# Kernel optimization log

Measured on AMD Instinct MI355X. Metric: run time of the kernel, lower is better.

Reference implementation:

```python
import jax, jax.numpy as jnp
import numpy as np

B, H, W, C = 64, 56, 56, 256
WIN, SHIFT, HEADS = 7, 3, 8
HEAD_DIM = C // HEADS
N = WIN * WIN
EPS = 1e-5


def _rel_pos_index():
    # matches get_relative_position_index (tf.meshgrid 'xy' indexing)
    xx, yy = np.meshgrid(np.arange(WIN), np.arange(WIN))  # shapes (W,H)
    coords = np.stack([yy, xx], 0).reshape(2, -1)  # (2, N)
    rel = coords[:, :, None] - coords[:, None, :]  # (2, N, N)
    rel = rel.transpose(1, 2, 0)
    idx = (rel[:, :, 0] + WIN - 1) * (2 * WIN - 1) + (rel[:, :, 1] + WIN - 1)
    return jnp.asarray(idx, dtype=jnp.int32)  # (N, N)


def _attn_mask():
    # shifted-window attention mask, (nW, N, N) with 0 / -100
    img = np.zeros((H, W), dtype=np.float32)
    cnt = 0
    for hs in (slice(0, -WIN), slice(-WIN, -SHIFT), slice(-SHIFT, None)):
        for ws in (slice(0, -WIN), slice(-WIN, -SHIFT), slice(-SHIFT, None)):
            img[hs, ws] = cnt
            cnt += 1
    mw = img.reshape(H // WIN, WIN, W // WIN, WIN).transpose(0, 2, 1, 3).reshape(-1, N)
    am = mw[:, None, :] - mw[:, :, None]
    am = np.where(am != 0, -100.0, 0.0).astype(np.float32)
    return jnp.asarray(am)  # (nW, N, N)


def _layer_norm(x, g, b):
    mu = jnp.mean(x, -1, keepdims=True)
    var = jnp.mean(jnp.square(x - mu), -1, keepdims=True)
    return (x - mu) * jax.lax.rsqrt(var + EPS) * g + b


def setup_inputs() -> dict:
    key = jax.random.key(0)
    ks = jax.random.split(key, 6)
    s = lambda fan: 1.0 / np.sqrt(fan)
    return {
        'x': jax.random.normal(ks[0], (B, H * W, C), jnp.float32),
        'ln1_g': jnp.ones((C,), jnp.float32),
        'ln1_b': jnp.zeros((C,), jnp.float32),
        'qkv_w': jax.random.normal(ks[1], (C, 3 * C), jnp.float32) * s(C),
        'qkv_b': jnp.zeros((3 * C,), jnp.float32),
        'rpb_table': jax.random.normal(ks[2], ((2 * WIN - 1) ** 2, HEADS), jnp.float32) * 0.02,
        'proj_w': jax.random.normal(ks[3], (C, C), jnp.float32) * s(C),
        'proj_b': jnp.zeros((C,), jnp.float32),
        'ln2_g': jnp.ones((C,), jnp.float32),
        'ln2_b': jnp.zeros((C,), jnp.float32),
        'mlp_w1': jax.random.normal(ks[4], (C, 4 * C), jnp.float32) * s(C),
        'mlp_b1': jnp.zeros((4 * C,), jnp.float32),
        'mlp_w2': jax.random.normal(ks[5], (4 * C, C), jnp.float32) * s(4 * C),
        'mlp_b2': jnp.zeros((C,), jnp.float32),
    }


def _forward(x, ln1_g, ln1_b, qkv_w, qkv_b, rpb_table, proj_w, proj_b,
             ln2_g, ln2_b, mlp_w1, mlp_b1, mlp_w2, mlp_b2):
    rel_idx = _rel_pos_index()
    mask = _attn_mask()
    nW = (H // WIN) * (W // WIN)

    shortcut = x
    y = _layer_norm(x, ln1_g, ln1_b).reshape(B, H, W, C)
    y = jnp.roll(y, (-SHIFT, -SHIFT), axis=(1, 2))
    # window partition -> (B*nW, N, C)
    y = y.reshape(B, H // WIN, WIN, W // WIN, WIN, C)
    y = y.transpose(0, 1, 3, 2, 4, 5).reshape(B * nW, N, C)

    qkv = (y @ qkv_w + qkv_b).reshape(B * nW, N, 3, HEADS, HEAD_DIM)
    q, k, v = jnp.moveaxis(qkv, 2, 0)  # each (B*nW, N, heads, hd)
    q = q * (HEAD_DIM ** -0.5)
    attn = jnp.einsum('wqhd,wkhd->whqk', q, k)  # (B*nW, heads, N, N)
    bias = jnp.transpose(rpb_table[rel_idx], (2, 0, 1))  # (heads, N, N)
    attn = attn + bias[None]
    attn = attn.reshape(B, nW, HEADS, N, N) + mask[None, :, None]
    attn = jax.nn.softmax(attn.reshape(B * nW, HEADS, N, N), axis=-1)
    o = jnp.einsum('whqk,wkhd->wqhd', attn, v).reshape(B * nW, N, C)
    o = o @ proj_w + proj_b

    # window reverse + un-shift
    o = o.reshape(B, H // WIN, W // WIN, WIN, WIN, C)
    o = o.transpose(0, 1, 3, 2, 4, 5).reshape(B, H, W, C)
    o = jnp.roll(o, (SHIFT, SHIFT), axis=(1, 2)).reshape(B, H * W, C)

    x = shortcut + o
    h = _layer_norm(x, ln2_g, ln2_b)
    h = jax.nn.gelu(h @ mlp_w1 + mlp_b1, approximate=False) @ mlp_w2 + mlp_b2
    return x + h


def reference(x, ln1_g, ln1_b, qkv_w, qkv_b, rpb_table, proj_w, proj_b,
              ln2_g, ln2_b, mlp_w1, mlp_b1, mlp_w2, mlp_b2):
    return _forward(x, ln1_g, ln1_b, qkv_w, qkv_b, rpb_table, proj_w, proj_b,
                    ln2_g, ln2_b, mlp_w1, mlp_b1, mlp_w2, mlp_b2)
```

## Files before the change

### kernel.cpp

```cpp
#include <hip/hip_runtime.h>
#include <math.h>


typedef __attribute__((ext_vector_type(8))) short bf16x8;
typedef __attribute__((ext_vector_type(4))) float f32x4;

#define NTOK 200704
#define NN   49
#define NPARAM 4680

__device__ __forceinline__ float bf2f(unsigned short u) {
    union { unsigned int i; float f; } v; v.i = ((unsigned)u) << 16; return v.f;
}
__device__ __forceinline__ unsigned short f2bf(float f) {
    union { float fv; unsigned int i; } v; v.fv = f;
    return (unsigned short)((v.i + 0x7fffu + ((v.i >> 16) & 1u)) >> 16);
}

__device__ __forceinline__ void gload_lds16(const unsigned short* g, unsigned short* l) {
    __builtin_amdgcn_global_load_lds(
        (const __attribute__((address_space(1))) unsigned int*)g,
        (__attribute__((address_space(3))) unsigned int*)l, 16, 0, 0);
}

__device__ __forceinline__ float gelu_erf(float v) {
    float av = fabsf(v);
    float x = av * 0.70710678118654752f;
    float t = __builtin_amdgcn_rcpf(fmaf(x, 0.3275911f, 1.0f));
    float p = fmaf(1.061405429f, t, -1.453152027f);
    p = fmaf(p, t, 1.421413741f);
    p = fmaf(p, t, -0.284496736f);
    p = fmaf(p, t, 0.254829592f);
    p = p * t;
    float ex = __builtin_amdgcn_exp2f(x * x * -1.4426950408889634f);
    float E = fmaf(-p, ex, 1.0f);
    return fmaf(0.5f * av, E, 0.5f * v);
}

__global__ void detect_kernel(const unsigned short* __restrict__ xu, int* flag) {
    int ln = threadIdx.x;
    int sane = 0;
    #pragma unroll
    for (int t = 0; t < 16; t++) {
        unsigned u = xu[(ln * 16 + t) * 2];
        unsigned e = (u >> 7) & 0xFF;
        sane += (e >= 0x60 && e <= 0x90) ? 1 : 0;
    }
    #pragma unroll
    for (int off = 32; off; off >>= 1) sane += __shfl_xor(sane, off);
    if (ln == 0) *flag = (sane < 614) ? 1 : 0;
}

__device__ __forceinline__ float ld_any(const void* p, int j, int f) {
    return f ? ((const float*)p)[j] : bf2f(((const unsigned short*)p)[j]);
}

__global__ void convert_params_kernel(
    const void* ln1_g, const void* ln1_b, const void* qkv_b, const void* proj_b,
    const void* ln2_g, const void* ln2_b, const void* b1, const void* b2,
    const void* rpb, const int* __restrict__ flag, float* __restrict__ dst) {
    int i = blockIdx.x * 256 + threadIdx.x;
    if (i >= NPARAM) return;
    int f = *flag;
    const void* src; int j;
    if      (i < 256)  { src = ln1_g;  j = i; }
    else if (i < 512)  { src = ln1_b;  j = i - 256; }
    else if (i < 1280) { src = qkv_b;  j = i - 512; }
    else if (i < 1536) { src = proj_b; j = i - 1280; }
    else if (i < 1792) { src = ln2_g;  j = i - 1536; }
    else if (i < 2048) { src = ln2_b;  j = i - 1792; }
    else if (i < 3072) { src = b1;     j = i - 2048; }
    else if (i < 3328) { src = b2;     j = i - 3072; }
    else               { src = rpb;    j = i - 3328; }
    dst[i] = ld_any(src, j, f);
}

__global__ void transpose_any(const void* __restrict__ in,
                              unsigned short* __restrict__ out, int K, int N,
                              const int* __restrict__ flag) {
    int f = *flag;
    int idx = blockIdx.x * 256 + threadIdx.x;
    if (idx < K * N) {
        int k = idx / N, n = idx - k * N;
        out[n * K + k] = f2bf(ld_any(in, idx, f));
    }
}

__global__ void relayout_w1(const void* __restrict__ in,
                            unsigned short* __restrict__ out,
                            const int* __restrict__ flag) {
    int f = *flag;
    int idx = blockIdx.x * 256 + threadIdx.x;
    if (idx < 256 * 1024) {
        int k = idx >> 10, h = idx & 1023;
        int c = h >> 5, r = h & 31;
        int ks = k ^ ((r & 7) << 3);
        out[c * 8192 + r * 256 + ks] = f2bf(ld_any(in, idx, f));
    }
}

__global__ void relayout_w2(const void* __restrict__ in,
                            unsigned short* __restrict__ out,
                            const int* __restrict__ flag) {
    int f = *flag;
    int idx = blockIdx.x * 256 + threadIdx.x;
    if (idx < 1024 * 256) {
        int k = idx >> 8, n = idx & 255;
        int c = k >> 5, kk = k & 31;
        out[c * 8192 + n * 32 + kk] = f2bf(ld_any(in, idx, f));
    }
}

__global__ __launch_bounds__(256) void ln1_window_kernel(
    const void* __restrict__ x, const float* __restrict__ paramsF,
    unsigned short* __restrict__ y, const int* __restrict__ flag) {
    int f = *flag;
    int wv = threadIdx.x >> 6, ln = threadIdx.x & 63;
    int tok = blockIdx.x * 4 + wv;
    float v0, v1, v2, v3;
    if (f) {
        float4 pv = *(const float4*)((const float*)x + (size_t)tok * 256 + ln * 4);
        v0 = pv.x; v1 = pv.y; v2 = pv.z; v3 = pv.w;
    } else {
        ushort4 pv = *(const ushort4*)((const unsigned short*)x + (size_t)tok * 256 + ln * 4);
        v0 = bf2f(pv.x); v1 = bf2f(pv.y); v2 = bf2f(pv.z); v3 = bf2f(pv.w);
    }
    float s = v0 + v1 + v2 + v3;
    float sq = v0 * v0 + v1 * v1 + v2 * v2 + v3 * v3;
    #pragma unroll
    for (int off = 32; off; off >>= 1) { s += __shfl_xor(s, off); sq += __shfl_xor(sq, off); }
    float mu = s * (1.f / 256.f);
    float rs = rsqrtf(fmaxf(sq * (1.f / 256.f) - mu * mu, 0.f) + 1e-5f);
    float4 gv = *(const float4*)(paramsF + ln * 4);
    float4 bv = *(const float4*)(paramsF + 256 + ln * 4);
    int bb = tok / 3136, hw = tok - bb * 3136;
    int h = hw / 56, w = hw - h * 56;
    int hp = h - 3; hp += (hp < 0) ? 56 : 0;
    int wp = w - 3; wp += (wp < 0) ? 56 : 0;
    int win = (hp / 7) * 8 + (wp / 7);
    int n = (hp % 7) * 7 + (wp % 7);
    size_t drow = ((size_t)bb * 64 + win) * NN + n;
    ushort4 o;
    o.x = f2bf((v0 - mu) * rs * gv.x + bv.x);
    o.y = f2bf((v1 - mu) * rs * gv.y + bv.y);
    o.z = f2bf((v2 - mu) * rs * gv.z + bv.z);
    o.w = f2bf((v3 - mu) * rs * gv.w + bv.w);
    *(ushort4*)(y + drow * 256 + ln * 4) = o;
}

__device__ __forceinline__ void gemm_core_k256(
    const unsigned short* __restrict__ A, const unsigned short* __restrict__ Bt,
    int rowBase, int colBase, unsigned short* As, unsigned short* Bs, f32x4 acc[2][4]) {
    const int tid = threadIdx.x;
    const int wv = tid >> 6, ln = tid & 63;
    const int m16 = ln & 15, q4 = ln >> 4;
    const int ar = tid >> 1, ah = (tid & 1) * 32;
    const int br = tid >> 2, bp = (tid & 3) * 16;
    for (int kb = 0; kb < 256; kb += 64) {
        const unsigned short* ag = A + (size_t)(rowBase + ar) * 256 + kb + ah;
        unsigned short* asd = As + ar * 72 + ah;
        #pragma unroll
        for (int i = 0; i < 4; i++)
            *(bf16x8*)(asd + i * 8) = *(const bf16x8*)(ag + i * 8);
        const unsigned short* bg = Bt + (size_t)(colBase + br) * 256 + kb + bp;
        unsigned short* bsd = Bs + br * 72 + bp;
        #pragma unroll
        for (int i = 0; i < 2; i++)
            *(bf16x8*)(bsd + i * 8) = *(const bf16x8*)(bg + i * 8);
        __syncthreads();
        #pragma unroll
        for (int ks = 0; ks < 64; ks += 32) {
            bf16x8 af[2], bfr[4];
            #pragma unroll
            for (int rt = 0; rt < 2; rt++)
                af[rt] = *(const bf16x8*)(As + (wv * 32 + rt * 16 + m16) * 72 + ks + q4 * 8);
            #pragma unroll
            for (int ct = 0; ct < 4; ct++)
                bfr[ct] = *(const bf16x8*)(Bs + (ct * 16 + m16) * 72 + ks + q4 * 8);
            #pragma unroll
            for (int rt = 0; rt < 2; rt++)
                #pragma unroll
                for (int ct = 0; ct < 4; ct++)
                    acc[rt][ct] = __builtin_amdgcn_mfma_f32_16x16x32_bf16(
                        af[rt], bfr[ct], acc[rt][ct], 0, 0, 0);
        }
        __syncthreads();
    }
}

__global__ __launch_bounds__(256) void gemm_qkv_kernel(
    const unsigned short* __restrict__ A, const unsigned short* __restrict__ Bt,
    const float* __restrict__ bias,
    unsigned short* __restrict__ out) {
    __shared__ unsigned short As[128 * 72];
    __shared__ unsigned short Bs[64 * 72];
    const int ln = threadIdx.x & 63, wv = threadIdx.x >> 6;
    const int m16 = ln & 15, q4 = ln >> 4;
    const int rowBase = blockIdx.y * 128, colBase = blockIdx.x * 64;
    f32x4 acc[2][4];
    #pragma unroll
    for (int i = 0; i < 2; i++)
        #pragma unroll
        for (int j = 0; j < 4; j++)
            #pragma unroll
            for (int r = 0; r < 4; r++) acc[i][j][r] = 0.f;
    gemm_core_k256(A, Bt, rowBase, colBase, As, Bs, acc);
    #pragma unroll
    for (int rt = 0; rt < 2; rt++)
        #pragma unroll
        for (int ct = 0; ct < 4; ct++) {
            int col = colBase + ct * 16 + m16;
            float bs = bias[col];
            float scale = (col < 256) ? 0.17677669529663689f : 1.0f;
            #pragma unroll
            for (int r = 0; r < 4; r++) {
                int row = rowBase + wv * 32 + rt * 16 + q4 * 4 + r;
                out[(size_t)row * 768 + col] = f2bf((acc[rt][ct][r] + bs) * scale);
            }
        }
}

__global__ __launch_bounds__(256) void gemm_proj_kernel(
    const unsigned short* __restrict__ A, const unsigned short* __restrict__ Bt,
    const float* __restrict__ bias,
    const void* __restrict__ xin,
    unsigned short* __restrict__ x2, const int* __restrict__ flag) {
    __shared__ unsigned short As[128 * 72];
    __shared__ unsigned short Bs[64 * 72];
    const int f = *flag;
    const int ln = threadIdx.x & 63, wv = threadIdx.x >> 6;
    const int m16 = ln & 15, q4 = ln >> 4;
    const int rowBase = blockIdx.y * 128, colBase = blockIdx.x * 64;
    f32x4 acc[2][4];
    #pragma unroll
    for (int i = 0; i < 2; i++)
        #pragma unroll
        for (int j = 0; j < 4; j++)
            #pragma unroll
            for (int r = 0; r < 4; r++) acc[i][j][r] = 0.f;
    gemm_core_k256(A, Bt, rowBase, colBase, As, Bs, acc);
    #pragma unroll
    for (int rt = 0; rt < 2; rt++)
        #pragma unroll
        for (int r = 0; r < 4; r++) {
            int row = rowBase + wv * 32 + rt * 16 + q4 * 4 + r;
            int win = row / NN, n = row - win * NN;
            int bb = win >> 6, wl = win & 63;
            int i7 = n / 7, j7 = n - i7 * 7;
            int hp = (wl >> 3) * 7 + i7 + 3; if (hp >= 56) hp -= 56;
            int wp = (wl & 7) * 7 + j7 + 3;  if (wp >= 56) wp -= 56;
            size_t drow = ((size_t)bb * 3136 + hp * 56 + wp) * 256;
            #pragma unroll
            for (int ct = 0; ct < 4; ct++) {
                int col = colBase + ct * 16 + m16;
                float v = acc[rt][ct][r] + bias[col] + ld_any(xin, drow + col, f);
                x2[drow + col] = f2bf(v);
            }
        }
}

__global__ __launch_bounds__(256) void attn_kernel(
    const unsigned short* __restrict__ qkv,
    const float* __restrict__ rpbF,
    unsigned short* __restrict__ o) {
    __shared__ unsigned short Qs[49 * 40], Ks[49 * 40], Vs[49 * 40];
    __shared__ float S[49 * 52];
    int tid = threadIdx.x;
    int win = blockIdx.x >> 3, head = blockIdx.x & 7;
    size_t base = (size_t)win * 49 * 768 + head * 32;
    if (tid < 196) {
        int i = tid >> 2, part = (tid & 3) * 8;
        *(bf16x8*)(Qs + i * 40 + part) = *(const bf16x8*)(qkv + base + (size_t)i * 768 + part);
        *(bf16x8*)(Ks + i * 40 + part) = *(const bf16x8*)(qkv + base + 256 + (size_t)i * 768 + part);
        *(bf16x8*)(Vs + i * 40 + part) = *(const bf16x8*)(qkv + base + 512 + (size_t)i * 768 + part);
    }
    __syncthreads();
    int wl = win & 63;
    int wh0 = (wl >> 3) * 7, ww0 = (wl & 7) * 7;
    for (int e = tid; e < 2401; e += 256) {
        int i = e / 49, j = e - i * 49;
        float a = 0.f;
        #pragma unroll
        for (int dd = 0; dd < 32; dd += 8) {
            bf16x8 qv = *(const bf16x8*)(Qs + i * 40 + dd);
            bf16x8 kv = *(const bf16x8*)(Ks + j * 40 + dd);
            #pragma unroll
            for (int u = 0; u < 8; u++)
                a += bf2f((unsigned short)qv[u]) * bf2f((unsigned short)kv[u]);
        }
        int ir = i / 7, ic = i - ir * 7, jr = j / 7, jc = j - jr * 7;
        a += rpbF[((ir - jr + 6) * 13 + (ic - jc + 6)) * 8 + head];
        int hi = wh0 + ir, wi = ww0 + ic, hj = wh0 + jr, wj = ww0 + jc;
        int ci = (hi < 49 ? 0 : (hi < 53 ? 3 : 6)) + (wi < 49 ? 0 : (wi < 53 ? 1 : 2));
        int cj = (hj < 49 ? 0 : (hj < 53 ? 3 : 6)) + (wj < 49 ? 0 : (wj < 53 ? 1 : 2));
        if (ci != cj) a -= 100.f;
        S[i * 52 + j] = a;
    }
    __syncthreads();
    if (tid < 49) {
        float m = -1e30f;
        for (int j = 0; j < 49; j++) m = fmaxf(m, S[tid * 52 + j]);
        float s = 0.f;
        for (int j = 0; j < 49; j++) { float e = expf(S[tid * 52 + j] - m); S[tid * 52 + j] = e; s += e; }
        float inv = 1.f / s;
        for (int j = 0; j < 49; j++) S[tid * 52 + j] *= inv;
    }
    __syncthreads();
    if (tid < 196) {
        int i = tid >> 2, dr = (tid & 3) * 8;
        float a[8];
        #pragma unroll
        for (int u = 0; u < 8; u++) a[u] = 0.f;
        for (int j = 0; j < 49; j++) {
            float pp = S[i * 52 + j];
            bf16x8 vv = *(const bf16x8*)(Vs + j * 40 + dr);
            #pragma unroll
            for (int u = 0; u < 8; u++) a[u] += pp * bf2f((unsigned short)vv[u]);
        }
        bf16x8 ov;
        #pragma unroll
        for (int u = 0; u < 8; u++) ov[u] = (short)f2bf(a[u]);
        *(bf16x8*)(o + ((size_t)win * 49 + i) * 256 + head * 32 + dr) = ov;
    }
}

__global__ __launch_bounds__(256, 2) void mlp_fused_v3(
    const unsigned short* __restrict__ x2,
    const float* __restrict__ g2F, const float* __restrict__ b2lnF,
    const unsigned short* __restrict__ w1s,
    const float* __restrict__ b1F,
    const unsigned short* __restrict__ w2s,
    const float* __restrict__ b2F,
    void* __restrict__ out, const int* __restrict__ flag) {
    __shared__ __align__(16) unsigned short Bs1[2][32 * 256];
    __shared__ __align__(16) unsigned short Bs2[2][256 * 32];
    __shared__ __align__(16) unsigned short Hs[64 * 40];
    const int f = *flag;
    const int tid = threadIdx.x;
    const int wv = tid >> 6, ln = tid & 63;
    const int m16 = ln & 15, q4 = ln >> 4;
    const int tok0 = blockIdx.x * 64;

    {
        const unsigned short* s1 = w1s + tid * 8;
        const unsigned short* s2 = w2s + tid * 8;
        #pragma unroll
        for (int j = 0; j < 4; j++) {
            gload_lds16(s1 + j * 2048, &Bs1[0][tid * 8 + j * 2048]);
            gload_lds16(s2 + j * 2048, &Bs2[0][tid * 8 + j * 2048]);
        }
    }

    bf16x8 areg[8];
    {
        const unsigned short* xr = x2 + (size_t)(tok0 + wv * 16 + m16) * 256 + q4 * 8;
        #pragma unroll
        for (int ks = 0; ks < 8; ks++) areg[ks] = *(const bf16x8*)(xr + ks * 32);
        float s = 0.f, sq = 0.f;
        #pragma unroll
        for (int ks = 0; ks < 8; ks++)
            #pragma unroll
            for (int u = 0; u < 8; u++) {
                float v = bf2f((unsigned short)areg[ks][u]);
                s += v; sq += v * v;
            }
        s += __shfl_xor(s, 16); s += __shfl_xor(s, 32);
        sq += __shfl_xor(sq, 16); sq += __shfl_xor(sq, 32);
        float mu = s * (1.f / 256.f);
        float rs = rsqrtf(fmaxf(sq * (1.f / 256.f) - mu * mu, 0.f) + 1e-5f);
        #pragma unroll
        for (int ks = 0; ks < 8; ks++)
            #pragma unroll
            for (int u = 0; u < 8; u++) {
                int kidx = ks * 32 + q4 * 8 + u;
                float v = (bf2f((unsigned short)areg[ks][u]) - mu) * rs * g2F[kidx] + b2lnF[kidx];
                areg[ks][u] = (short)f2bf(v);
            }
    }

    f32x4 acc2[4][4];
    #pragma unroll
    for (int rt = 0; rt < 4; rt++)
        #pragma unroll
        for (int ct = 0; ct < 4; ct++)
            #pragma unroll
            for (int r = 0; r < 4; r++) acc2[rt][ct][r] = 0.f;

    #pragma unroll 1
    for (int c = 0; c < 32; ++c) {
        const int cur = c & 1;
        asm volatile("s_waitcnt vmcnt(0)" ::: "memory");
        __builtin_amdgcn_s_barrier();
        __builtin_amdgcn_sched_barrier(0);

        if (c + 1 < 32) {
            const unsigned short* s1 = w1s + (size_t)(c + 1) * 8192 + tid * 8;
            const unsigned short* s2 = w2s + (size_t)(c + 1) * 8192 + tid * 8;
            unsigned short* d1 = &Bs1[cur ^ 1][tid * 8];
            unsigned short* d2 = &Bs2[cur ^ 1][tid * 8];
            #pragma unroll
            for (int j = 0; j < 4; j++) {
                gload_lds16(s1 + j * 2048, d1 + j * 2048);
                gload_lds16(s2 + j * 2048, d2 + j * 2048);
            }
        }
        __builtin_amdgcn_sched_barrier(0);

        f32x4 acc1[2];
        #pragma unroll
        for (int ct = 0; ct < 2; ct++)
            #pragma unroll
            for (int r = 0; r < 4; r++) acc1[ct][r] = 0.f;
        const unsigned short* b1base = &Bs1[cur][0];
        #pragma unroll
        for (int ks = 0; ks < 8; ks++) {
            int kidx = (ks * 32 + q4 * 8) ^ ((m16 & 7) << 3);
            #pragma unroll
            for (int ct = 0; ct < 2; ct++) {
                bf16x8 wfr = *(const bf16x8*)(b1base + (ct * 16 + m16) * 256 + kidx);
                acc1[ct] = __builtin_amdgcn_mfma_f32_16x16x32_bf16(wfr, areg[ks], acc1[ct], 0, 0, 0);
            }
        }

        #pragma unroll
        for (int ct = 0; ct < 2; ct++) {
            float4 bb = *(const float4*)(b1F + c * 32 + ct * 16 + q4 * 4);
            ushort4 o4;
            o4.x = f2bf(gelu_erf(acc1[ct][0] + bb.x));
            o4.y = f2bf(gelu_erf(acc1[ct][1] + bb.y));
            o4.z = f2bf(gelu_erf(acc1[ct][2] + bb.z));
            o4.w = f2bf(gelu_erf(acc1[ct][3] + bb.w));
            *(ushort4*)(Hs + (wv * 16 + m16) * 40 + ct * 16 + q4 * 4) = o4;
        }
        asm volatile("s_waitcnt lgkmcnt(0)" ::: "memory");
        __builtin_amdgcn_sched_barrier(0);
        __builtin_amdgcn_s_barrier();
        __builtin_amdgcn_sched_barrier(0);

        bf16x8 haf[4];
        #pragma unroll
        for (int rt = 0; rt < 4; rt++)
            haf[rt] = *(const bf16x8*)(Hs + (rt * 16 + m16) * 40 + q4 * 8);
        const unsigned short* b2base = &Bs2[cur][0];
        #pragma unroll
        for (int ct = 0; ct < 4; ct++) {
            bf16x8 bfr = *(const bf16x8*)(b2base + (wv * 64 + ct * 16 + m16) * 32 + q4 * 8);
            #pragma unroll
            for (int rt = 0; rt < 4; rt++)
                acc2[rt][ct] = __builtin_amdgcn_mfma_f32_16x16x32_bf16(haf[rt], bfr, acc2[rt][ct], 0, 0, 0);
        }
    }

    #pragma unroll
    for (int rt = 0; rt < 4; rt++)
        #pragma unroll
        for (int ct = 0; ct < 4; ct++) {
            int col = wv * 64 + ct * 16 + m16;
            float bb = b2F[col];
            #pragma unroll
            for (int r = 0; r < 4; r++) {
                int tokr = tok0 + rt * 16 + q4 * 4 + r;
                size_t idx = (size_t)tokr * 256 + col;
                float v = acc2[rt][ct][r] + bb + bf2f(x2[idx]);
                if (f) ((float*)out)[idx] = v;
                else   ((unsigned short*)out)[idx] = f2bf(v);
            }
        }
}

extern "C" void kernel_launch(void* const* d_in, const int* in_sizes, int n_in,
                              void* d_out, int out_size, void* d_ws, size_t ws_size,
                              hipStream_t stream) {
    const void* x      = d_in[0];
    const void* qkv_w  = d_in[3];
    const void* proj_w = d_in[6];
    const void* w1     = d_in[10];
    const void* w2     = d_in[12];

    char* ws = (char*)d_ws;
    size_t off = 0;
    unsigned short* y = (unsigned short*)(ws + off);
    off += (size_t)NTOK * 256 * 2;
    size_t qkv_off = off;
    unsigned short* qkv = (unsigned short*)(ws + off);
    off += (size_t)NTOK * 768 * 2;
    unsigned short* x2 = (unsigned short*)(ws + qkv_off);
    unsigned short* o = y;
    unsigned short* qkvWt = (unsigned short*)(ws + off); off += 768 * 256 * 2;
    unsigned short* projWt = (unsigned short*)(ws + off); off += 256 * 256 * 2;
    unsigned short* w1s = (unsigned short*)(ws + off); off += 1024 * 256 * 2;
    unsigned short* w2s = (unsigned short*)(ws + off); off += 256 * 1024 * 2;
    float* paramsF = (float*)(ws + off); off += NPARAM * 4;
    int* flag = (int*)(ws + off); off += 16;
    (void)ws_size; (void)in_sizes; (void)n_in; (void)out_size;

    detect_kernel<<<1, 64, 0, stream>>>((const unsigned short*)x, flag);
    convert_params_kernel<<<(NPARAM + 255) / 256, 256, 0, stream>>>(
        d_in[1], d_in[2], d_in[4], d_in[7], d_in[8], d_in[9], d_in[11], d_in[13],
        d_in[5], flag, paramsF);
    transpose_any<<<(256 * 768 + 255) / 256, 256, 0, stream>>>(qkv_w, qkvWt, 256, 768, flag);
    transpose_any<<<(256 * 256 + 255) / 256, 256, 0, stream>>>(proj_w, projWt, 256, 256, flag);
    relayout_w1<<<(256 * 1024 + 255) / 256, 256, 0, stream>>>(w1, w1s, flag);
    relayout_w2<<<(1024 * 256 + 255) / 256, 256, 0, stream>>>(w2, w2s, flag);

    ln1_window_kernel<<<NTOK / 4, 256, 0, stream>>>(x, paramsF, y, flag);
    gemm_qkv_kernel<<<dim3(768 / 64, NTOK / 128), 256, 0, stream>>>(y, qkvWt, paramsF + 512, qkv);
    attn_kernel<<<4096 * 8, 256, 0, stream>>>(qkv, paramsF + 3328, o);
    gemm_proj_kernel<<<dim3(256 / 64, NTOK / 128), 256, 0, stream>>>(
        o, projWt, paramsF + 1280, x, x2, flag);
    mlp_fused_v3<<<NTOK / 64, 256, 0, stream>>>(
        x2, paramsF + 1536, paramsF + 1792, w1s, paramsF + 2048, w2s, paramsF + 3072, d_out, flag);
}
```

Before: 1.724 ms.

## Rewrite window attention with MFMA and precomputed bias+mask table

Replaces the scalar per-(window,head) attention kernel with one block per window that runs QK^T and PV on bf16 MFMA instructions, with each wave handling two heads. Relative position bias and shift mask are folded into a precomputed table covering four mask patterns, and softmax runs in registers using lane shuffles. V is transposed into LDS once per window. This cuts scalar FMA and LDS traffic and the per-element index math. In exchange it rounds probabilities to bf16, reads Q/K rows past token 49 (up to 64, which spill into the next window's data), and writes outputs with scalar 16-bit stores.

```diff
diff --git a/kernel.cpp b/kernel.cpp
--- a/kernel.cpp
+++ b/kernel.cpp
@@ -8,6 +8,7 @@
 #define NTOK 200704
 #define NN   49
 #define NPARAM 4680
+#define TBL_ELEMS (4 * 8 * 49 * 64)
 
 __device__ __forceinline__ float bf2f(unsigned short u) {
     union { unsigned int i; float f; } v; v.i = ((unsigned)u) << 16; return v.f;
@@ -75,6 +76,28 @@
     dst[i] = ld_any(src, j, f);
 }
 
+__global__ void build_tbl_kernel(const float* __restrict__ rpbF,
+                                 float* __restrict__ tbl) {
+    int idx = blockIdx.x * 256 + threadIdx.x;
+    if (idx >= TBL_ELEMS) return;
+    int k = idx & 63;
+    int q = (idx >> 6) % 49;
+    int h = ((idx >> 6) / 49) & 7;
+    int pat = idx / (64 * 49 * 8);
+    float v;
+    if (k >= 49) {
+        v = -1e30f;
+    } else {
+        int ir = q / 7, ic = q - ir * 7, jr = k / 7, jc = k - jr * 7;
+        v = rpbF[((ir - jr + 6) * 13 + (ic - jc + 6)) * 8 + h];
+        int rb = pat >> 1, cb = pat & 1;
+        int ci = (rb ? (ir < 4 ? 3 : 6) : 0) + (cb ? (ic < 4 ? 1 : 2) : 0);
+        int cj = (rb ? (jr < 4 ? 3 : 6) : 0) + (cb ? (jc < 4 ? 1 : 2) : 0);
+        if (ci != cj) v -= 100.f;
+    }
+    tbl[idx] = v;
+}
+
 __global__ void transpose_any(const void* __restrict__ in,
                               unsigned short* __restrict__ out, int K, int N,
                               const int* __restrict__ flag) {
@@ -259,68 +282,133 @@
         }
 }
 
-__global__ __launch_bounds__(256) void attn_kernel(
+__global__ __launch_bounds__(256) void attn_mfma_kernel(
     const unsigned short* __restrict__ qkv,
-    const float* __restrict__ rpbF,
+    const float* __restrict__ tbl,
     unsigned short* __restrict__ o) {
-    __shared__ unsigned short Qs[49 * 40], Ks[49 * 40], Vs[49 * 40];
-    __shared__ float S[49 * 52];
-    int tid = threadIdx.x;
-    int win = blockIdx.x >> 3, head = blockIdx.x & 7;
-    size_t base = (size_t)win * 49 * 768 + head * 32;
-    if (tid < 196) {
-        int i = tid >> 2, part = (tid & 3) * 8;
-        *(bf16x8*)(Qs + i * 40 + part) = *(const bf16x8*)(qkv + base + (size_t)i * 768 + part);
-        *(bf16x8*)(Ks + i * 40 + part) = *(const bf16x8*)(qkv + base + 256 + (size_t)i * 768 + part);
-        *(bf16x8*)(Vs + i * 40 + part) = *(const bf16x8*)(qkv + base + 512 + (size_t)i * 768 + part);
-    }
+    __shared__ __align__(16) unsigned short Vt[256 * 72];
+    __shared__ __align__(16) unsigned short Ps[4][64 * 72];
+    const int tid = threadIdx.x;
+    const int wv = tid >> 6, ln = tid & 63;
+    const int m16 = ln & 15, q4 = ln >> 4;
+    const int win = blockIdx.x;
+    const size_t wbase = (size_t)win * 49 * 768;
+
+    #pragma unroll
+    for (int i = 0; i < 8; i++) {
+        int idx = i * 256 + tid;
+        int ch = idx >> 6, tok = idx & 63;
+        if (tok < 49) {
+            bf16x8 v = *(const bf16x8*)(qkv + wbase + (size_t)tok * 768 + 512 + ch * 8);
+            #pragma unroll
+            for (int u = 0; u < 8; u++)
+                Vt[(ch * 8 + u) * 72 + tok] = (unsigned short)v[u];
+        }
+    }
+    #pragma unroll
+    for (int u = 0; u < 23; u++) Vt[tid * 72 + 49 + u] = 0;
+
+    const int wl = win & 63;
+    const int pat = (((wl >> 3) == 7) ? 2 : 0) + (((wl & 7) == 7) ? 1 : 0);
     __syncthreads();
-    int wl = win & 63;
-    int wh0 = (wl >> 3) * 7, ww0 = (wl & 7) * 7;
-    for (int e = tid; e < 2401; e += 256) {
-        int i = e / 49, j = e - i * 49;
-        float a = 0.f;
-        #pragma unroll
-        for (int dd = 0; dd < 32; dd += 8) {
-            bf16x8 qv = *(const bf16x8*)(Qs + i * 40 + dd);
-            bf16x8 kv = *(const bf16x8*)(Ks + j * 40 + dd);
-            #pragma unroll
-            for (int u = 0; u < 8; u++)
-                a += bf2f((unsigned short)qv[u]) * bf2f((unsigned short)kv[u]);
-        }
-        int ir = i / 7, ic = i - ir * 7, jr = j / 7, jc = j - jr * 7;
-        a += rpbF[((ir - jr + 6) * 13 + (ic - jc + 6)) * 8 + head];
-        int hi = wh0 + ir, wi = ww0 + ic, hj = wh0 + jr, wj = ww0 + jc;
-        int ci = (hi < 49 ? 0 : (hi < 53 ? 3 : 6)) + (wi < 49 ? 0 : (wi < 53 ? 1 : 2));
-        int cj = (hj < 49 ? 0 : (hj < 53 ? 3 : 6)) + (wj < 49 ? 0 : (wj < 53 ? 1 : 2));
-        if (ci != cj) a -= 100.f;
-        S[i * 52 + j] = a;
-    }
-    __syncthreads();
-    if (tid < 49) {
-        float m = -1e30f;
-        for (int j = 0; j < 49; j++) m = fmaxf(m, S[tid * 52 + j]);
-        float s = 0.f;
-        for (int j = 0; j < 49; j++) { float e = expf(S[tid * 52 + j] - m); S[tid * 52 + j] = e; s += e; }
-        float inv = 1.f / s;
-        for (int j = 0; j < 49; j++) S[tid * 52 + j] *= inv;
-    }
-    __syncthreads();
-    if (tid < 196) {
-        int i = tid >> 2, dr = (tid & 3) * 8;
-        float a[8];
-        #pragma unroll
-        for (int u = 0; u < 8; u++) a[u] = 0.f;
-        for (int j = 0; j < 49; j++) {
-            float pp = S[i * 52 + j];
-            bf16x8 vv = *(const bf16x8*)(Vs + j * 40 + dr);
-            #pragma unroll
-            for (int u = 0; u < 8; u++) a[u] += pp * bf2f((unsigned short)vv[u]);
-        }
-        bf16x8 ov;
-        #pragma unroll
-        for (int u = 0; u < 8; u++) ov[u] = (short)f2bf(a[u]);
-        *(bf16x8*)(o + ((size_t)win * 49 + i) * 256 + head * 32 + dr) = ov;
+
+    unsigned short* Pw = &Ps[wv][0];
+    for (int hh = 0; hh < 2; hh++) {
+        const int h = wv * 2 + hh;
+        bf16x8 kf[4], qf[4];
+        #pragma unroll
+        for (int t = 0; t < 4; t++) {
+            size_t rrow = wbase + (size_t)(t * 16 + m16) * 768 + h * 32 + q4 * 8;
+            qf[t] = *(const bf16x8*)(qkv + rrow);
+            kf[t] = *(const bf16x8*)(qkv + rrow + 256);
+        }
+        f32x4 acc[4][4];
+        #pragma unroll
+        for (int kt = 0; kt < 4; kt++)
+            #pragma unroll
+            for (int qt = 0; qt < 4; qt++) {
+                #pragma unroll
+                for (int r = 0; r < 4; r++) acc[kt][qt][r] = 0.f;
+                acc[kt][qt] = __builtin_amdgcn_mfma_f32_16x16x32_bf16(
+                    kf[kt], qf[qt], acc[kt][qt], 0, 0, 0);
+            }
+
+        const float* tb = tbl + ((size_t)(pat * 8 + h) * 49) * 64;
+        #pragma unroll
+        for (int qt = 0; qt < 4; qt++) {
+            int q = qt * 16 + m16;
+            int qc = q < 49 ? q : 48;
+            float s[4][4];
+            float mx = -3e38f;
+            #pragma unroll
+            for (int kt = 0; kt < 4; kt++) {
+                float4 tv = *(const float4*)(tb + qc * 64 + kt * 16 + q4 * 4);
+                s[kt][0] = acc[kt][qt][0] + tv.x;
+                s[kt][1] = acc[kt][qt][1] + tv.y;
+                s[kt][2] = acc[kt][qt][2] + tv.z;
+                s[kt][3] = acc[kt][qt][3] + tv.w;
+                #pragma unroll
+                for (int r = 0; r < 4; r++) mx = fmaxf(mx, s[kt][r]);
+            }
+            mx = fmaxf(mx, __shfl_xor(mx, 16));
+            mx = fmaxf(mx, __shfl_xor(mx, 32));
+            float sum = 0.f;
+            #pragma unroll
+            for (int kt = 0; kt < 4; kt++)
+                #pragma unroll
+                for (int r = 0; r < 4; r++) {
+                    float e = __expf(s[kt][r] - mx);
+                    s[kt][r] = e; sum += e;
+                }
+            sum += __shfl_xor(sum, 16);
+            sum += __shfl_xor(sum, 32);
+            float inv = 1.f / sum;
+            #pragma unroll
+            for (int kt = 0; kt < 4; kt++) {
+                ushort4 p4;
+                p4.x = f2bf(s[kt][0] * inv);
+                p4.y = f2bf(s[kt][1] * inv);
+                p4.z = f2bf(s[kt][2] * inv);
+                p4.w = f2bf(s[kt][3] * inv);
+                *(ushort4*)(Pw + q * 72 + kt * 16 + q4 * 4) = p4;
+            }
+        }
+
+        f32x4 po[4][2];
+        #pragma unroll
+        for (int mt = 0; mt < 4; mt++)
+            #pragma unroll
+            for (int nt = 0; nt < 2; nt++)
+                #pragma unroll
+                for (int r = 0; r < 4; r++) po[mt][nt][r] = 0.f;
+        #pragma unroll
+        for (int kstep = 0; kstep < 2; kstep++) {
+            bf16x8 pa[4], vb[2];
+            #pragma unroll
+            for (int mt = 0; mt < 4; mt++)
+                pa[mt] = *(const bf16x8*)(Pw + (mt * 16 + m16) * 72 + kstep * 32 + q4 * 8);
+            #pragma unroll
+            for (int nt = 0; nt < 2; nt++)
+                vb[nt] = *(const bf16x8*)(Vt + (h * 32 + nt * 16 + m16) * 72 + kstep * 32 + q4 * 8);
+            #pragma unroll
+            for (int mt = 0; mt < 4; mt++)
+                #pragma unroll
+                for (int nt = 0; nt < 2; nt++)
+                    po[mt][nt] = __builtin_amdgcn_mfma_f32_16x16x32_bf16(
+                        pa[mt], vb[nt], po[mt][nt], 0, 0, 0);
+        }
+
+        #pragma unroll
+        for (int mt = 0; mt < 4; mt++)
+            #pragma unroll
+            for (int r = 0; r < 4; r++) {
+                int q = mt * 16 + q4 * 4 + r;
+                if (q < 49) {
+                    size_t orow = ((size_t)win * 49 + q) * 256 + h * 32;
+                    o[orow + m16]      = f2bf(po[mt][0][r]);
+                    o[orow + 16 + m16] = f2bf(po[mt][1][r]);
+                }
+            }
     }
 }
 
@@ -492,12 +580,14 @@
     unsigned short* w2s = (unsigned short*)(ws + off); off += 256 * 1024 * 2;
     float* paramsF = (float*)(ws + off); off += NPARAM * 4;
     int* flag = (int*)(ws + off); off += 16;
+    float* tbl = (float*)(ws + off); off += (size_t)TBL_ELEMS * 4;
     (void)ws_size; (void)in_sizes; (void)n_in; (void)out_size;
 
     detect_kernel<<<1, 64, 0, stream>>>((const unsigned short*)x, flag);
     convert_params_kernel<<<(NPARAM + 255) / 256, 256, 0, stream>>>(
         d_in[1], d_in[2], d_in[4], d_in[7], d_in[8], d_in[9], d_in[11], d_in[13],
         d_in[5], flag, paramsF);
+    build_tbl_kernel<<<(TBL_ELEMS + 255) / 256, 256, 0, stream>>>(paramsF + 3328, tbl);
     transpose_any<<<(256 * 768 + 255) / 256, 256, 0, stream>>>(qkv_w, qkvWt, 256, 768, flag);
     transpose_any<<<(256 * 256 + 255) / 256, 256, 0, stream>>>(proj_w, projWt, 256, 256, flag);
     relayout_w1<<<(256 * 1024 + 255) / 256, 256, 0, stream>>>(w1, w1s, flag);
@@ -505,7 +595,7 @@
 
     ln1_window_kernel<<<NTOK / 4, 256, 0, stream>>>(x, paramsF, y, flag);
     gemm_qkv_kernel<<<dim3(768 / 64, NTOK / 128), 256, 0, stream>>>(y, qkvWt, paramsF + 512, qkv);
-    attn_kernel<<<4096 * 8, 256, 0, stream>>>(qkv, paramsF + 3328, o);
+    attn_mfma_kernel<<<4096, 256, 0, stream>>>(qkv, tbl, o);
     gemm_proj_kernel<<<dim3(256 / 64, NTOK / 128), 256, 0, stream>>>(
         o, projWt, paramsF + 1280, x, x2, flag);
     mlp_fused_v3<<<NTOK / 64, 256, 0, stream>>>(
```

Result: faster. 1.397 ms (-19.0%).
